# Optimization experiments

Measured on AMD Instinct MI355X. Metric: run time of the kernel, lower is better.

Reference implementation:

```python
import jax, jax.numpy as jnp
import numpy as np

V, E, F, K, Y = 50000, 128, 256, 3, 1000  # vocab, embed, filters, kernel, labels


def setup_inputs() -> dict:
    key = jax.random.key(0)
    ks = jax.random.split(key, 8)
    x = jax.random.randint(ks[0], (16, 4096), 0, V)
    target = jax.random.randint(ks[1], (16,), 0, Y)
    embed_w = jax.random.normal(ks[2], (V, E), dtype=jnp.float32) * 0.02
    embed_w = embed_w.at[0].set(0.0)  # padding_idx=0
    conv_w = jax.random.normal(ks[3], (F, E, K), dtype=jnp.float32) * (1.0 / np.sqrt(E * K))
    conv_b = jnp.zeros((F,), dtype=jnp.float32)
    U_w = jax.random.normal(ks[4], (Y, F), dtype=jnp.float32) * (1.0 / np.sqrt(F))
    fc_w = jax.random.normal(ks[5], (Y, F), dtype=jnp.float32) * (1.0 / np.sqrt(F))
    fc_b = jnp.zeros((Y,), dtype=jnp.float32)
    return {"x": x, "target": target, "embed_w": embed_w, "conv_w": conv_w,
            "conv_b": conv_b, "U_w": U_w, "fc_w": fc_w, "fc_b": fc_b}


def reference(x, target, embed_w, conv_w, conv_b, U_w, fc_w, fc_b):
    # embedding lookup: (B, L, E); dropout is identity in eval mode
    h = embed_w[x]
    h = jnp.transpose(h, (0, 2, 1))  # (B, E, L)
    # conv1d, SAME padding (pad = floor(K/2) = 1 for K=3)
    h = jax.lax.conv_general_dilated(
        h, conv_w, window_strides=(1,), padding="SAME",
        dimension_numbers=("NCH", "OIH", "NCH"))
    h = jax.nn.relu(h + conv_b[None, :, None])  # (B, F, L)
    # label-wise attention: scores (B, Y, L), softmax over L
    scores = jnp.einsum("yf,bfl->byl", U_w, h)
    alpha = jax.nn.softmax(scores, axis=2)
    # attend: m (B, Y, F)
    m = jnp.einsum("byl,bfl->byf", alpha, h)
    # per-label dot with fc rows + bias -> logits (B, Y)
    logit = jnp.sum(fc_w[None] * m, axis=2) + fc_b
    # cross-entropy loss (target='drg')
    logp = jax.nn.log_softmax(logit, axis=1)
    loss = -jnp.mean(jnp.take_along_axis(logp, target[:, None], axis=1))
    return (logit, loss)
```

## Files before the change

### kernel.cpp

```cpp
#include <hip/hip_runtime.h>
#include <math.h>

using short8  = __attribute__((ext_vector_type(8))) short;
using floatx4 = __attribute__((ext_vector_type(4))) float;
using uintx4  = __attribute__((ext_vector_type(4))) unsigned int;
using uintx2  = __attribute__((ext_vector_type(2))) unsigned int;

#define AS1 __attribute__((address_space(1)))
#define AS3 __attribute__((address_space(3)))

__device__ __forceinline__ unsigned short f2bf(float f) {
  union { float f; unsigned int u; } v; v.f = f;
  unsigned int r = v.u + 0x7FFFu + ((v.u >> 16) & 1u);
  return (unsigned short)(r >> 16);
}
__device__ __forceinline__ float bf2f(unsigned short h) {
  union { unsigned int u; float f; } v; v.u = ((unsigned int)h) << 16;
  return v.f;
}
__device__ __forceinline__ void gload_lds16(const void* g, void* l) {
  __builtin_amdgcn_global_load_lds((const AS1 unsigned int*)g, (AS3 unsigned int*)l, 16, 0, 0);
}

#define B_  16
#define L_  4096
#define E_  128
#define F_  256
#define Y_  1000

#define OFF_HLF   0u
#define OFF_HFL   33554432u
#define OFF_UBF   67108864u
#define OFF_WBF   67633152u
#define OFF_PART  67829760u
#define OFF_LOSST 68354048u

__global__ __launch_bounds__(256) void k_repack_u(const float* __restrict__ Uw,
                                                  unsigned short* __restrict__ ubf) {
  int i = blockIdx.x * 256 + threadIdx.x;
  int y = i >> 8, f = i & 255;
  float v = (y < Y_) ? Uw[y * F_ + f] : 0.f;
  ubf[i] = f2bf(v);
}

__global__ __launch_bounds__(256) void k_repack_w(const float* __restrict__ cw,
                                                  unsigned short* __restrict__ wbf) {
  int i = blockIdx.x * 256 + threadIdx.x;
  const float* s = cw + (size_t)i * 3;
  wbf[0 * 32768 + i] = f2bf(s[0]);
  wbf[1 * 32768 + i] = f2bf(s[1]);
  wbf[2 * 32768 + i] = f2bf(s[2]);
}

#define ET_STR 272
#define TT_STR 144
__global__ __launch_bounds__(256, 4) void k_conv(const unsigned short* __restrict__ wbf,
                                                 const float* __restrict__ conv_b,
                                                 const int* __restrict__ x,
                                                 const float* __restrict__ ew,
                                                 unsigned short* __restrict__ hlf,
                                                 unsigned short* __restrict__ hfl) {
  __shared__ unsigned char lds[66 * ET_STR + 2 * 64 * TT_STR];
  unsigned char* et = lds;
  unsigned char* tl = lds + 66 * ET_STR;
  unsigned char* tf = tl + 64 * TT_STR;
  const int tid = threadIdx.x, bid = blockIdx.x;
  const int b = bid >> 6, l0 = (bid & 63) << 6;
  const int w = tid >> 6, lane = tid & 63, c = lane & 15, q = lane >> 4;
  const int* xb = x + b * L_;
  for (int s = tid; s < 1056; s += 256) {
    int row = s >> 4, sg = s & 15;
    int l = l0 - 1 + row;
    int idx = (l >= 0 && l < L_) ? xb[l] : 0;
    const float4* src = (const float4*)(ew + (size_t)idx * E_ + sg * 8);
    float4 a = src[0], bb = src[1];
    uintx4 v;
    v.x = (unsigned int)f2bf(a.x) | ((unsigned int)f2bf(a.y) << 16);
    v.y = (unsigned int)f2bf(a.z) | ((unsigned int)f2bf(a.w) << 16);
    v.z = (unsigned int)f2bf(bb.x) | ((unsigned int)f2bf(bb.y) << 16);
    v.w = (unsigned int)f2bf(bb.z) | ((unsigned int)f2bf(bb.w) << 16);
    *(uintx4*)(et + row * ET_STR + sg * 16) = v;
  }
  __syncthreads();
  for (int nq = 0; nq < 4; ++nq) {
    const int fg = nq * 64 + w * 16 + c;
    short8 wf[3][4];
    #pragma unroll
    for (int d = 0; d < 3; ++d)
      #pragma unroll
      for (int kq = 0; kq < 4; ++kq)
        wf[d][kq] = *(const short8*)((const unsigned char*)wbf +
                      ((size_t)(d * F_ + fg) * E_ + kq * 32 + q * 8) * 2);
    const float bias = conv_b[fg];
    floatx4 acc[4];
    #pragma unroll
    for (int ms = 0; ms < 4; ++ms) acc[ms] = (floatx4){0.f, 0.f, 0.f, 0.f};
    #pragma unroll
    for (int d = 0; d < 3; ++d)
      #pragma unroll
      for (int kq = 0; kq < 4; ++kq)
        #pragma unroll
        for (int ms = 0; ms < 4; ++ms) {
          short8 a = *(const short8*)(et + (ms * 16 + c + d) * ET_STR + kq * 64 + q * 16);
          acc[ms] = __builtin_amdgcn_mfma_f32_16x16x32_bf16(a, wf[d][kq], acc[ms], 0, 0, 0);
        }
    const int fl = w * 16 + c;
    #pragma unroll
    for (int ms = 0; ms < 4; ++ms)
      #pragma unroll
      for (int r = 0; r < 4; ++r) {
        float v = acc[ms][r] + bias;
        v = v > 0.f ? v : 0.f;
        unsigned short h = f2bf(v);
        int ll = ms * 16 + q * 4 + r;
        *(unsigned short*)(tl + ll * TT_STR + fl * 2) = h;
        *(unsigned short*)(tf + fl * TT_STR + ll * 2) = h;
      }
    __syncthreads();
    for (int s = tid; s < 512; s += 256) {
      int row = s >> 3, sg = s & 7;
      *(uintx4*)((unsigned char*)hlf + (((size_t)b * L_ + l0 + row) * F_ + nq * 64 + sg * 8) * 2) =
          *(const uintx4*)(tl + row * TT_STR + sg * 16);
    }
    for (int s = tid; s < 512; s += 256) {
      int fr = s >> 3, sg = s & 7;
      *(uintx4*)((unsigned char*)hfl + (((size_t)b * F_ + nq * 64 + fr) * L_ + l0 + sg * 8) * 2) =
          *(const uintx4*)(tf + fr * TT_STR + sg * 16);
    }
    __syncthreads();
  }
}

__global__ __launch_bounds__(256, 2) void k_attn(const unsigned short* __restrict__ ubf,
                                                 const unsigned short* __restrict__ hlf,
                                                 const unsigned short* __restrict__ hfl,
                                                 const float* __restrict__ fcw,
                                                 float2* __restrict__ part) {
  __shared__ unsigned char lds[75776];
  unsigned char* sP = lds + 65536;
  const int tid = threadIdx.x;
  const int w = tid >> 6, lane = tid & 63, c = lane & 15, q = lane >> 4;
  const int bid = blockIdx.x;
  const int xcd = bid & 7, r0 = bid >> 3;
  const int b = xcd * 2 + (r0 & 1);
  const int r2 = r0 >> 1, yt = r2 & 7, chunk = r2 >> 3;
  const int y0 = yt << 7;
  short8 uf[2][8];
  #pragma unroll
  for (int mt = 0; mt < 2; ++mt)
    #pragma unroll
    for (int kq = 0; kq < 8; ++kq)
      uf[mt][kq] = *(const short8*)((const unsigned char*)ubf +
                     ((size_t)(y0 + w * 32 + mt * 16 + c) * F_ + kq * 32 + q * 8) * 2);
  floatx4 O[16][2];
  #pragma unroll
  for (int mt = 0; mt < 16; ++mt) {
    O[mt][0] = (floatx4){0.f, 0.f, 0.f, 0.f};
    O[mt][1] = (floatx4){0.f, 0.f, 0.f, 0.f};
  }
  float Lacc[2][4] = {{0.f,0.f,0.f,0.f},{0.f,0.f,0.f,0.f}};
  const unsigned char* hlfb = (const unsigned char*)hlf + (size_t)b * L_ * (F_ * 2);
  const unsigned char* hflb = (const unsigned char*)hfl + (size_t)b * F_ * (L_ * 2);
  int boff[8];
  #pragma unroll
  for (int kq = 0; kq < 8; ++kq) boff[kq] = c * 512 + (((kq * 4 + q) ^ (c & 7)) << 4);
  const int aoffc = c * 64 + ((q ^ (c & 3)) << 4);
  const int pw_base = (w * 32 + q * 4) * 80 + c * 2;
  const int pr_base = (w * 32 + c) * 80 + q * 16;
  const int sl_r = lane >> 5, sl_g = lane & 31;
  const int sf_r = lane >> 2, sf_g = lane & 3;
  const int l0base = chunk << 10;

#define STAGE(dstbuf, l0v)                                                      \
  {                                                                             \
    unsigned char* dstb = (dstbuf);                                             \
    _Pragma("unroll")                                                           \
    for (int ii = 0; ii < 4; ++ii) {                                            \
      int i = w * 4 + ii;                                                       \
      int r = 2 * i + sl_r;                                                     \
      int g = sl_g ^ (r & 7);                                                   \
      gload_lds16(hlfb + (size_t)((l0v) + r) * 512 + g * 16, dstb + i * 1024);  \
    }                                                                           \
    _Pragma("unroll")                                                           \
    for (int ii = 0; ii < 4; ++ii) {                                            \
      int i = w * 4 + ii;                                                       \
      int r = 16 * i + sf_r;                                                    \
      int g = sf_g ^ (r & 3);                                                   \
      gload_lds16(hflb + (size_t)r * 8192 + (size_t)(l0v) * 2 + g * 16,         \
                  dstb + 16384 + i * 1024);                                     \
    }                                                                           \
  }

  STAGE(lds, l0base);
  __syncthreads();
  for (int it = 0; it < 32; ++it) {
    unsigned char* curb = lds + ((it & 1) << 15);
    if (it < 31) {
      unsigned char* nxtb = lds + (((it & 1) ^ 1) << 15);
      STAGE(nxtb, l0base + (it + 1) * 32);
    }
    unsigned char* shlf = curb;
    unsigned char* shfl = curb + 16384;
    floatx4 S[2][2];
    S[0][0] = (floatx4){0.f,0.f,0.f,0.f}; S[0][1] = (floatx4){0.f,0.f,0.f,0.f};
    S[1][0] = (floatx4){0.f,0.f,0.f,0.f}; S[1][1] = (floatx4){0.f,0.f,0.f,0.f};
    #pragma unroll
    for (int kq = 0; kq < 8; ++kq)
      #pragma unroll
      for (int nt = 0; nt < 2; ++nt) {
        short8 bb = *(const short8*)(shlf + nt * 8192 + boff[kq]);
        S[0][nt] = __builtin_amdgcn_mfma_f32_16x16x32_bf16(uf[0][kq], bb, S[0][nt], 0, 0, 0);
        S[1][nt] = __builtin_amdgcn_mfma_f32_16x16x32_bf16(uf[1][kq], bb, S[1][nt], 0, 0, 0);
      }
    #pragma unroll
    for (int mt = 0; mt < 2; ++mt)
      #pragma unroll
      for (int nt = 0; nt < 2; ++nt)
        #pragma unroll
        for (int r = 0; r < 4; ++r) {
          float p = __expf(S[mt][nt][r]);
          unsigned short h = f2bf(p);
          *(unsigned short*)(sP + pw_base + mt * 1280 + r * 80 + nt * 32) = h;
          Lacc[mt][r] += bf2f(h);
        }
    short8 bp0 = *(const short8*)(sP + pr_base);
    short8 bp1 = *(const short8*)(sP + pr_base + 1280);
    #pragma unroll
    for (int mt = 0; mt < 16; ++mt) {
      short8 a = *(const short8*)(shfl + mt * 1024 + aoffc);
      O[mt][0] = __builtin_amdgcn_mfma_f32_16x16x32_bf16(a, bp0, O[mt][0], 0, 0, 0);
      O[mt][1] = __builtin_amdgcn_mfma_f32_16x16x32_bf16(a, bp1, O[mt][1], 0, 0, 0);
    }
    __syncthreads();
  }
  #pragma unroll
  for (int mt = 0; mt < 2; ++mt)
    #pragma unroll
    for (int r = 0; r < 4; ++r) {
      float v = Lacc[mt][r];
      v += __shfl_xor(v, 1, 64); v += __shfl_xor(v, 2, 64);
      v += __shfl_xor(v, 4, 64); v += __shfl_xor(v, 8, 64);
      Lacc[mt][r] = v;
    }
  float num[2];
  #pragma unroll
  for (int nt = 0; nt < 2; ++nt) {
    int ya = y0 + w * 32 + nt * 16 + c;
    float s = 0.f;
    if (ya < Y_) {
      const float* fr = fcw + (size_t)ya * F_;
      #pragma unroll
      for (int mt = 0; mt < 16; ++mt)
        #pragma unroll
        for (int r = 0; r < 4; ++r)
          s += O[mt][nt][r] * fr[mt * 16 + q * 4 + r];
    }
    s += __shfl_xor(s, 16, 64); s += __shfl_xor(s, 32, 64);
    num[nt] = s;
  }
  float2* pb = part + (size_t)((b * 8 + yt) * 4 + chunk) * 128;
  if (q == 0) {
    #pragma unroll
    for (int nt = 0; nt < 2; ++nt) pb[w * 32 + nt * 16 + c].x = num[nt];
  }
  if (c == 0) {
    #pragma unroll
    for (int mt = 0; mt < 2; ++mt)
      #pragma unroll
      for (int r = 0; r < 4; ++r) pb[w * 32 + mt * 16 + q * 4 + r].y = Lacc[mt][r];
  }
}

__global__ __launch_bounds__(256) void k_logits(const float2* __restrict__ part,
                                                const float* __restrict__ fcb,
                                                const int* __restrict__ target,
                                                float* __restrict__ out,
                                                float* __restrict__ losst) {
  __shared__ float red[4];
  const int b = blockIdx.x, tid = threadIdx.x;
  const int w = tid >> 6;
  float lg[4];
  #pragma unroll
  for (int k = 0; k < 4; ++k) {
    int y = tid + k * 256;
    int yt = y >> 7, yl = y & 127;
    float n = 0.f, la = 0.f;
    #pragma unroll
    for (int ch = 0; ch < 4; ++ch) {
      float2 v = part[(size_t)((b * 8 + yt) * 4 + ch) * 128 + yl];
      n += v.x; la += v.y;
    }
    float lv = (y < Y_) ? (n / la + fcb[y]) : -1e30f;
    lg[k] = lv;
    if (y < Y_) out[b * Y_ + y] = lv;
  }
  float m = fmaxf(fmaxf(lg[0], lg[1]), fmaxf(lg[2], lg[3]));
  for (int off = 1; off < 64; off <<= 1) m = fmaxf(m, __shfl_xor(m, off, 64));
  if ((tid & 63) == 0) red[w] = m;
  __syncthreads();
  m = fmaxf(fmaxf(red[0], red[1]), fmaxf(red[2], red[3]));
  __syncthreads();
  float s = 0.f;
  #pragma unroll
  for (int k = 0; k < 4; ++k)
    if (tid + k * 256 < Y_) s += __expf(lg[k] - m);
  for (int off = 1; off < 64; off <<= 1) s += __shfl_xor(s, off, 64);
  if ((tid & 63) == 0) red[w] = s;
  __syncthreads();
  s = red[0] + red[1] + red[2] + red[3];
  int t = target[b];
  #pragma unroll
  for (int k = 0; k < 4; ++k)
    if (tid + k * 256 == t) losst[b] = -(lg[k] - m - logf(s));
}

__global__ __launch_bounds__(64) void k_sum(const float* __restrict__ losst,
                                            float* __restrict__ out) {
  int lane = threadIdx.x;
  float v = (lane < B_) ? losst[lane] : 0.f;
  v += __shfl_xor(v, 1, 64); v += __shfl_xor(v, 2, 64);
  v += __shfl_xor(v, 4, 64); v += __shfl_xor(v, 8, 64);
  if (lane == 0) out[B_ * Y_] = v * (1.f / (float)B_);
}

extern "C" void kernel_launch(void* const* d_in, const int* in_sizes, int n_in,
                              void* d_out, int out_size, void* d_ws, size_t ws_size,
                              hipStream_t stream) {
  const int*   x       = (const int*)d_in[0];
  const int*   target  = (const int*)d_in[1];
  const float* embed_w = (const float*)d_in[2];
  const float* conv_w  = (const float*)d_in[3];
  const float* conv_b  = (const float*)d_in[4];
  const float* U_w     = (const float*)d_in[5];
  const float* fc_w    = (const float*)d_in[6];
  const float* fc_b    = (const float*)d_in[7];
  float* out = (float*)d_out;
  unsigned char* ws = (unsigned char*)d_ws;
  unsigned short* hlf   = (unsigned short*)(ws + OFF_HLF);
  unsigned short* hfl   = (unsigned short*)(ws + OFF_HFL);
  unsigned short* ubf   = (unsigned short*)(ws + OFF_UBF);
  unsigned short* wbf   = (unsigned short*)(ws + OFF_WBF);
  float2*         part  = (float2*)(ws + OFF_PART);
  float*          losst = (float*)(ws + OFF_LOSST);

  k_repack_u<<<1024, 256, 0, stream>>>(U_w, ubf);
  k_repack_w<<<128, 256, 0, stream>>>(conv_w, wbf);
  k_conv<<<1024, 256, 0, stream>>>(wbf, conv_b, x, embed_w, hlf, hfl);
  k_attn<<<512, 256, 0, stream>>>(ubf, hlf, hfl, fc_w, part);
  k_logits<<<16, 256, 0, stream>>>(part, fc_b, target, out, losst);
  k_sum<<<1, 64, 0, stream>>>(losst, out);
}
```

Measured before the change: 198.4 us.

## Fold fc projection into attention via per-position fc·h scores, drop transposed h

Computes fc_w·h per position with a second MFMA alongside the attention scores, so each label accumulates sum(exp(s)*g) and sum(exp(s)) directly instead of building the full attended F-vector. This removes the transposed h copy written by the conv kernel and the P-through-LDS second GEMM, cutting memory traffic and LDS use. The conv kernel also drops its LDS transpose staging and writes h directly with scalar 2-byte stores, which may be less coalesced. fc_w is now rounded to bf16, slightly changing numerics.

Result: faster. 185.7 us (-6.4%).

```diff
diff --git a/kernel.cpp b/kernel.cpp
--- a/kernel.cpp
+++ b/kernel.cpp
@@ -1,10 +1,10 @@
 #include <hip/hip_runtime.h>
 #include <math.h>
 
-using short8  = __attribute__((ext_vector_type(8))) short;
-using floatx4 = __attribute__((ext_vector_type(4))) float;
-using uintx4  = __attribute__((ext_vector_type(4))) unsigned int;
-using uintx2  = __attribute__((ext_vector_type(2))) unsigned int;
+using short8   = __attribute__((ext_vector_type(8)))  short;
+using floatx4  = __attribute__((ext_vector_type(4)))  float;
+using floatx16 = __attribute__((ext_vector_type(16))) float;
+using uintx4   = __attribute__((ext_vector_type(4)))  unsigned int;
 
 #define AS1 __attribute__((address_space(1)))
 #define AS3 __attribute__((address_space(3)))
@@ -13,10 +13,6 @@
   union { float f; unsigned int u; } v; v.f = f;
   unsigned int r = v.u + 0x7FFFu + ((v.u >> 16) & 1u);
   return (unsigned short)(r >> 16);
-}
-__device__ __forceinline__ float bf2f(unsigned short h) {
-  union { unsigned int u; float f; } v; v.u = ((unsigned int)h) << 16;
-  return v.f;
 }
 __device__ __forceinline__ void gload_lds16(const void* g, void* l) {
   __builtin_amdgcn_global_load_lds((const AS1 unsigned int*)g, (AS3 unsigned int*)l, 16, 0, 0);
@@ -29,18 +25,18 @@
 #define Y_  1000
 
 #define OFF_HLF   0u
-#define OFF_HFL   33554432u
-#define OFF_UBF   67108864u
-#define OFF_WBF   67633152u
-#define OFF_PART  67829760u
-#define OFF_LOSST 68354048u
-
-__global__ __launch_bounds__(256) void k_repack_u(const float* __restrict__ Uw,
-                                                  unsigned short* __restrict__ ubf) {
+#define OFF_UBF   33554432u
+#define OFF_FBF   34078720u
+#define OFF_WBF   34603008u
+#define OFF_PART  34799616u
+#define OFF_LOSST 35323904u
+
+__global__ __launch_bounds__(256) void k_repack_u(const float* __restrict__ src,
+                                                  unsigned short* __restrict__ dst) {
   int i = blockIdx.x * 256 + threadIdx.x;
   int y = i >> 8, f = i & 255;
-  float v = (y < Y_) ? Uw[y * F_ + f] : 0.f;
-  ubf[i] = f2bf(v);
+  float v = (y < Y_) ? src[y * F_ + f] : 0.f;
+  dst[i] = f2bf(v);
 }
 
 __global__ __launch_bounds__(256) void k_repack_w(const float* __restrict__ cw,
@@ -53,17 +49,12 @@
 }
 
 #define ET_STR 272
-#define TT_STR 144
 __global__ __launch_bounds__(256, 4) void k_conv(const unsigned short* __restrict__ wbf,
                                                  const float* __restrict__ conv_b,
                                                  const int* __restrict__ x,
                                                  const float* __restrict__ ew,
-                                                 unsigned short* __restrict__ hlf,
-                                                 unsigned short* __restrict__ hfl) {
-  __shared__ unsigned char lds[66 * ET_STR + 2 * 64 * TT_STR];
-  unsigned char* et = lds;
-  unsigned char* tl = lds + 66 * ET_STR;
-  unsigned char* tf = tl + 64 * TT_STR;
+                                                 unsigned short* __restrict__ hlf) {
+  __shared__ unsigned char et[66 * ET_STR];
   const int tid = threadIdx.x, bid = blockIdx.x;
   const int b = bid >> 6, l0 = (bid & 63) << 6;
   const int w = tid >> 6, lane = tid & 63, c = lane & 15, q = lane >> 4;
@@ -82,93 +73,70 @@
     *(uintx4*)(et + row * ET_STR + sg * 16) = v;
   }
   __syncthreads();
-  for (int nq = 0; nq < 4; ++nq) {
-    const int fg = nq * 64 + w * 16 + c;
-    short8 wf[3][4];
-    #pragma unroll
-    for (int d = 0; d < 3; ++d)
-      #pragma unroll
-      for (int kq = 0; kq < 4; ++kq)
-        wf[d][kq] = *(const short8*)((const unsigned char*)wbf +
-                      ((size_t)(d * F_ + fg) * E_ + kq * 32 + q * 8) * 2);
-    const float bias = conv_b[fg];
-    floatx4 acc[4];
-    #pragma unroll
-    for (int ms = 0; ms < 4; ++ms) acc[ms] = (floatx4){0.f, 0.f, 0.f, 0.f};
-    #pragma unroll
-    for (int d = 0; d < 3; ++d)
-      #pragma unroll
-      for (int kq = 0; kq < 4; ++kq)
+  const int fw = w * 64;
+  floatx4 acc[4][4];
+  #pragma unroll
+  for (int ms = 0; ms < 4; ++ms)
+    #pragma unroll
+    for (int nt = 0; nt < 4; ++nt) acc[ms][nt] = (floatx4){0.f, 0.f, 0.f, 0.f};
+  #pragma unroll
+  for (int d = 0; d < 3; ++d)
+    #pragma unroll
+    for (int kq = 0; kq < 4; ++kq) {
+      short8 aa[4], bb[4];
+      #pragma unroll
+      for (int ms = 0; ms < 4; ++ms)
+        aa[ms] = *(const short8*)(et + (ms * 16 + q * 4 + (0) + c * 0 + 0 + (ms * 0)) * 0 +
+                                  (ms * 16 + c + d) * ET_STR + kq * 64 + q * 16);
+      #pragma unroll
+      for (int nt = 0; nt < 4; ++nt)
+        bb[nt] = *(const short8*)((const unsigned char*)wbf +
+                   ((size_t)(d * F_ + fw + nt * 16 + c) * E_ + kq * 32 + q * 8) * 2);
+      #pragma unroll
+      for (int ms = 0; ms < 4; ++ms)
         #pragma unroll
-        for (int ms = 0; ms < 4; ++ms) {
-          short8 a = *(const short8*)(et + (ms * 16 + c + d) * ET_STR + kq * 64 + q * 16);
-          acc[ms] = __builtin_amdgcn_mfma_f32_16x16x32_bf16(a, wf[d][kq], acc[ms], 0, 0, 0);
-        }
-    const int fl = w * 16 + c;
+        for (int nt = 0; nt < 4; ++nt)
+          acc[ms][nt] = __builtin_amdgcn_mfma_f32_16x16x32_bf16(aa[ms], bb[nt], acc[ms][nt], 0, 0, 0);
+    }
+  #pragma unroll
+  for (int nt = 0; nt < 4; ++nt) {
+    int f = fw + nt * 16 + c;
+    float bias = conv_b[f];
     #pragma unroll
     for (int ms = 0; ms < 4; ++ms)
       #pragma unroll
       for (int r = 0; r < 4; ++r) {
-        float v = acc[ms][r] + bias;
+        int l = l0 + ms * 16 + q * 4 + r;
+        float v = acc[ms][nt][r] + bias;
         v = v > 0.f ? v : 0.f;
-        unsigned short h = f2bf(v);
-        int ll = ms * 16 + q * 4 + r;
-        *(unsigned short*)(tl + ll * TT_STR + fl * 2) = h;
-        *(unsigned short*)(tf + fl * TT_STR + ll * 2) = h;
+        hlf[((size_t)b * L_ + l) * F_ + f] = f2bf(v);
       }
-    __syncthreads();
-    for (int s = tid; s < 512; s += 256) {
-      int row = s >> 3, sg = s & 7;
-      *(uintx4*)((unsigned char*)hlf + (((size_t)b * L_ + l0 + row) * F_ + nq * 64 + sg * 8) * 2) =
-          *(const uintx4*)(tl + row * TT_STR + sg * 16);
-    }
-    for (int s = tid; s < 512; s += 256) {
-      int fr = s >> 3, sg = s & 7;
-      *(uintx4*)((unsigned char*)hfl + (((size_t)b * F_ + nq * 64 + fr) * L_ + l0 + sg * 8) * 2) =
-          *(const uintx4*)(tf + fr * TT_STR + sg * 16);
-    }
-    __syncthreads();
   }
 }
 
 __global__ __launch_bounds__(256, 2) void k_attn(const unsigned short* __restrict__ ubf,
+                                                 const unsigned short* __restrict__ fbf,
                                                  const unsigned short* __restrict__ hlf,
-                                                 const unsigned short* __restrict__ hfl,
-                                                 const float* __restrict__ fcw,
                                                  float2* __restrict__ part) {
-  __shared__ unsigned char lds[75776];
-  unsigned char* sP = lds + 65536;
+  __shared__ unsigned char lds[32768];
   const int tid = threadIdx.x;
-  const int w = tid >> 6, lane = tid & 63, c = lane & 15, q = lane >> 4;
+  const int w = tid >> 6, lane = tid & 63, lo = lane & 31, hi = lane >> 5;
   const int bid = blockIdx.x;
   const int xcd = bid & 7, r0 = bid >> 3;
   const int b = xcd * 2 + (r0 & 1);
   const int r2 = r0 >> 1, yt = r2 & 7, chunk = r2 >> 3;
-  const int y0 = yt << 7;
-  short8 uf[2][8];
-  #pragma unroll
-  for (int mt = 0; mt < 2; ++mt)
-    #pragma unroll
-    for (int kq = 0; kq < 8; ++kq)
-      uf[mt][kq] = *(const short8*)((const unsigned char*)ubf +
-                     ((size_t)(y0 + w * 32 + mt * 16 + c) * F_ + kq * 32 + q * 8) * 2);
-  floatx4 O[16][2];
-  #pragma unroll
-  for (int mt = 0; mt < 16; ++mt) {
-    O[mt][0] = (floatx4){0.f, 0.f, 0.f, 0.f};
-    O[mt][1] = (floatx4){0.f, 0.f, 0.f, 0.f};
-  }
-  float Lacc[2][4] = {{0.f,0.f,0.f,0.f},{0.f,0.f,0.f,0.f}};
+  const int y0 = yt << 7, yw = y0 + w * 32;
+  short8 uf[16], ff[16];
+  #pragma unroll
+  for (int ks = 0; ks < 16; ++ks) {
+    size_t off = ((size_t)(yw + lo) * F_ + ks * 16 + hi * 8) * 2;
+    uf[ks] = *(const short8*)((const unsigned char*)ubf + off);
+    ff[ks] = *(const short8*)((const unsigned char*)fbf + off);
+  }
+  float num[16], den[16];
+  #pragma unroll
+  for (int r = 0; r < 16; ++r) { num[r] = 0.f; den[r] = 0.f; }
   const unsigned char* hlfb = (const unsigned char*)hlf + (size_t)b * L_ * (F_ * 2);
-  const unsigned char* hflb = (const unsigned char*)hfl + (size_t)b * F_ * (L_ * 2);
-  int boff[8];
-  #pragma unroll
-  for (int kq = 0; kq < 8; ++kq) boff[kq] = c * 512 + (((kq * 4 + q) ^ (c & 7)) << 4);
-  const int aoffc = c * 64 + ((q ^ (c & 3)) << 4);
-  const int pw_base = (w * 32 + q * 4) * 80 + c * 2;
-  const int pr_base = (w * 32 + c) * 80 + q * 16;
-  const int sl_r = lane >> 5, sl_g = lane & 31;
-  const int sf_r = lane >> 2, sf_g = lane & 3;
   const int l0base = chunk << 10;
 
 #define STAGE(dstbuf, l0v)                                                      \
@@ -177,97 +145,51 @@
     _Pragma("unroll")                                                           \
     for (int ii = 0; ii < 4; ++ii) {                                            \
       int i = w * 4 + ii;                                                       \
-      int r = 2 * i + sl_r;                                                     \
-      int g = sl_g ^ (r & 7);                                                   \
+      int r = 2 * i + hi;                                                       \
+      int g = lo ^ r;                                                           \
       gload_lds16(hlfb + (size_t)((l0v) + r) * 512 + g * 16, dstb + i * 1024);  \
     }                                                                           \
-    _Pragma("unroll")                                                           \
-    for (int ii = 0; ii < 4; ++ii) {                                            \
-      int i = w * 4 + ii;                                                       \
-      int r = 16 * i + sf_r;                                                    \
-      int g = sf_g ^ (r & 3);                                                   \
-      gload_lds16(hflb + (size_t)r * 8192 + (size_t)(l0v) * 2 + g * 16,         \
-                  dstb + 16384 + i * 1024);                                     \
-    }                                                                           \
   }
 
   STAGE(lds, l0base);
   __syncthreads();
   for (int it = 0; it < 32; ++it) {
-    unsigned char* curb = lds + ((it & 1) << 15);
-    if (it < 31) {
-      unsigned char* nxtb = lds + (((it & 1) ^ 1) << 15);
-      STAGE(nxtb, l0base + (it + 1) * 32);
-    }
-    unsigned char* shlf = curb;
-    unsigned char* shfl = curb + 16384;
-    floatx4 S[2][2];
-    S[0][0] = (floatx4){0.f,0.f,0.f,0.f}; S[0][1] = (floatx4){0.f,0.f,0.f,0.f};
-    S[1][0] = (floatx4){0.f,0.f,0.f,0.f}; S[1][1] = (floatx4){0.f,0.f,0.f,0.f};
-    #pragma unroll
-    for (int kq = 0; kq < 8; ++kq)
-      #pragma unroll
-      for (int nt = 0; nt < 2; ++nt) {
-        short8 bb = *(const short8*)(shlf + nt * 8192 + boff[kq]);
-        S[0][nt] = __builtin_amdgcn_mfma_f32_16x16x32_bf16(uf[0][kq], bb, S[0][nt], 0, 0, 0);
-        S[1][nt] = __builtin_amdgcn_mfma_f32_16x16x32_bf16(uf[1][kq], bb, S[1][nt], 0, 0, 0);
-      }
-    #pragma unroll
-    for (int mt = 0; mt < 2; ++mt)
-      #pragma unroll
-      for (int nt = 0; nt < 2; ++nt)
-        #pragma unroll
-        for (int r = 0; r < 4; ++r) {
-          float p = __expf(S[mt][nt][r]);
-          unsigned short h = f2bf(p);
-          *(unsigned short*)(sP + pw_base + mt * 1280 + r * 80 + nt * 32) = h;
-          Lacc[mt][r] += bf2f(h);
-        }
-    short8 bp0 = *(const short8*)(sP + pr_base);
-    short8 bp1 = *(const short8*)(sP + pr_base + 1280);
-    #pragma unroll
-    for (int mt = 0; mt < 16; ++mt) {
-      short8 a = *(const short8*)(shfl + mt * 1024 + aoffc);
-      O[mt][0] = __builtin_amdgcn_mfma_f32_16x16x32_bf16(a, bp0, O[mt][0], 0, 0, 0);
-      O[mt][1] = __builtin_amdgcn_mfma_f32_16x16x32_bf16(a, bp1, O[mt][1], 0, 0, 0);
+    unsigned char* cur = lds + ((it & 1) << 14);
+    if (it < 31) STAGE(lds + (((it & 1) ^ 1) << 14), l0base + (it + 1) * 32);
+    floatx16 S = {0.f,0.f,0.f,0.f,0.f,0.f,0.f,0.f,0.f,0.f,0.f,0.f,0.f,0.f,0.f,0.f};
+    floatx16 G = {0.f,0.f,0.f,0.f,0.f,0.f,0.f,0.f,0.f,0.f,0.f,0.f,0.f,0.f,0.f,0.f};
+    #pragma unroll
+    for (int ks = 0; ks < 16; ++ks) {
+      short8 bb = *(const short8*)(cur + lo * 512 + (((ks * 2 + hi) ^ lo) << 4));
+      S = __builtin_amdgcn_mfma_f32_32x32x16_bf16(uf[ks], bb, S, 0, 0, 0);
+      G = __builtin_amdgcn_mfma_f32_32x32x16_bf16(ff[ks], bb, G, 0, 0, 0);
+    }
+    #pragma unroll
+    for (int r = 0; r < 16; ++r) {
+      float p = __expf(S[r]);
+      num[r] += p * G[r];
+      den[r] += p;
     }
     __syncthreads();
   }
   #pragma unroll
-  for (int mt = 0; mt < 2; ++mt)
-    #pragma unroll
-    for (int r = 0; r < 4; ++r) {
-      float v = Lacc[mt][r];
-      v += __shfl_xor(v, 1, 64); v += __shfl_xor(v, 2, 64);
-      v += __shfl_xor(v, 4, 64); v += __shfl_xor(v, 8, 64);
-      Lacc[mt][r] = v;
-    }
-  float num[2];
-  #pragma unroll
-  for (int nt = 0; nt < 2; ++nt) {
-    int ya = y0 + w * 32 + nt * 16 + c;
-    float s = 0.f;
-    if (ya < Y_) {
-      const float* fr = fcw + (size_t)ya * F_;
-      #pragma unroll
-      for (int mt = 0; mt < 16; ++mt)
-        #pragma unroll
-        for (int r = 0; r < 4; ++r)
-          s += O[mt][nt][r] * fr[mt * 16 + q * 4 + r];
-    }
-    s += __shfl_xor(s, 16, 64); s += __shfl_xor(s, 32, 64);
-    num[nt] = s;
+  for (int r = 0; r < 16; ++r) {
+    float n = num[r], d = den[r];
+    n += __shfl_xor(n, 1, 64);  d += __shfl_xor(d, 1, 64);
+    n += __shfl_xor(n, 2, 64);  d += __shfl_xor(d, 2, 64);
+    n += __shfl_xor(n, 4, 64);  d += __shfl_xor(d, 4, 64);
+    n += __shfl_xor(n, 8, 64);  d += __shfl_xor(d, 8, 64);
+    n += __shfl_xor(n, 16, 64); d += __shfl_xor(d, 16, 64);
+    num[r] = n; den[r] = d;
   }
   float2* pb = part + (size_t)((b * 8 + yt) * 4 + chunk) * 128;
-  if (q == 0) {
-    #pragma unroll
-    for (int nt = 0; nt < 2; ++nt) pb[w * 32 + nt * 16 + c].x = num[nt];
-  }
-  if (c == 0) {
-    #pragma unroll
-    for (int mt = 0; mt < 2; ++mt)
-      #pragma unroll
-      for (int r = 0; r < 4; ++r) pb[w * 32 + mt * 16 + q * 4 + r].y = Lacc[mt][r];
+  if (lo == 0) {
+    #pragma unroll
+    for (int r = 0; r < 16; ++r) {
+      int yl = w * 32 + (r & 3) + 8 * (r >> 2) + 4 * hi;
+      float2 v; v.x = num[r]; v.y = den[r];
+      pb[yl] = v;
+    }
   }
 }
 
@@ -337,16 +259,17 @@
   float* out = (float*)d_out;
   unsigned char* ws = (unsigned char*)d_ws;
   unsigned short* hlf   = (unsigned short*)(ws + OFF_HLF);
-  unsigned short* hfl   = (unsigned short*)(ws + OFF_HFL);
   unsigned short* ubf   = (unsigned short*)(ws + OFF_UBF);
+  unsigned short* fbf   = (unsigned short*)(ws + OFF_FBF);
   unsigned short* wbf   = (unsigned short*)(ws + OFF_WBF);
   float2*         part  = (float2*)(ws + OFF_PART);
   float*          losst = (float*)(ws + OFF_LOSST);
 
   k_repack_u<<<1024, 256, 0, stream>>>(U_w, ubf);
+  k_repack_u<<<1024, 256, 0, stream>>>(fc_w, fbf);
   k_repack_w<<<128, 256, 0, stream>>>(conv_w, wbf);
-  k_conv<<<1024, 256, 0, stream>>>(wbf, conv_b, x, embed_w, hlf, hfl);
-  k_attn<<<512, 256, 0, stream>>>(ubf, hlf, hfl, fc_w, part);
+  k_conv<<<1024, 256, 0, stream>>>(wbf, conv_b, x, embed_w, hlf);
+  k_attn<<<512, 256, 0, stream>>>(ubf, fbf, hlf, part);
   k_logits<<<16, 256, 0, stream>>>(part, fc_b, target, out, losst);
   k_sum<<<1, 64, 0, stream>>>(losst, out);
 }
```
